# Performance work log

Hardware: AMD Instinct MI355X
Metric: run time of the kernel (lower is better)

Reference implementation:

```python
import jax, jax.numpy as jnp
import numpy as np

D = 3            # sheaf stalk dimension
HID = 128        # hidden_channels
OUT_SHAPE = (3, 3)
N_ROWS = 60000   # N_nodes * D
E = 960000       # edges (divisible by D)


def setup_inputs() -> dict:
    key = jax.random.key(0)
    k1, k2, k3 = jax.random.split(key, 3)
    x = jax.random.normal(k1, (N_ROWS, HID), dtype=jnp.float32)
    # nn.Linear(2*HID, prod(out_shape), bias=False): weight [out, in]
    W = jax.random.normal(k2, (int(np.prod(OUT_SHAPE)), 2 * HID), dtype=jnp.float32) * (1.0 / np.sqrt(2 * HID))
    edge_index = jax.random.randint(k3, (2, E), 0, N_ROWS, dtype=jnp.int64)
    return {"x": x, "W": W, "edge_index": edge_index}


def reference(x, W, edge_index):
    row, col = edge_index[0], edge_index[1]
    x_row = x[row]                                   # [E, HID] gather
    x_col = x[col]                                   # [E, HID] gather
    x_cat = jnp.concatenate([x_row, x_col], axis=-1) # [E, 2*HID]
    x_cat = x_cat.reshape(-1, D, 2 * HID).sum(axis=1)  # [E//D, 2*HID]
    maps = jnp.tanh(x_cat @ W.T)                     # [E//D, prod(out_shape)]
    return maps.reshape(-1, OUT_SHAPE[0], OUT_SHAPE[1])
```

## Files before the change

### kernel.cpp

```cpp
#include <hip/hip_runtime.h>
#include <hip/hip_fp16.h>
#include <math.h>

#define DD       3
#define HID      128
#define NOUT     9
#define N_ROWS_C 60000
#define NEDGE    960000
#define NGROUP   (NEDGE / DD)
#define YH_STRIDE 32

template <int CTRL>
__device__ __forceinline__ float dpp_xor_add(float v) {
    int r = __builtin_amdgcn_update_dpp(0, __float_as_int(v), CTRL, 0xf, 0xf, true);
    return v + __int_as_float(r);
}
__device__ __forceinline__ float red8(float v) {
    v = dpp_xor_add<0xB1>(v);
    v = dpp_xor_add<0x4E>(v);
    v = dpp_xor_add<0x141>(v);
    return v;
}

__device__ __forceinline__ float fast_tanh(float v) {
    float e = __builtin_amdgcn_exp2f(v * 2.8853900817779268f);
    return 1.0f - 2.0f * __builtin_amdgcn_rcpf(e + 1.0f);
}

__device__ __forceinline__ unsigned int pk(float a, float b) {
    __half2 h = __floats2half2_rn(a, b);
    return *reinterpret_cast<unsigned int*>(&h);
}

__global__ __launch_bounds__(256) void precompute_y(
    const float* __restrict__ x, const float* __restrict__ W, __half* __restrict__ yh)
{
    __shared__ float4 sW[576];
    const int t = threadIdx.x;
    const float4* __restrict__ Wv = reinterpret_cast<const float4*>(W);
    for (int i = t; i < 576; i += 256) sW[i] = Wv[i];

    const int s    = t & 7;
    const int slot = t >> 3;
    const int base = blockIdx.x * 64;
    const int r0   = base + slot;
    const int r1   = base + 32 + slot;
    const int r1c  = (r1 < N_ROWS_C) ? r1 : 0;

    __syncthreads();

    const float4* __restrict__ xv = reinterpret_cast<const float4*>(x);

    float aL0[NOUT], aR0[NOUT], aL1[NOUT], aR1[NOUT];
#pragma unroll
    for (int j = 0; j < NOUT; ++j) { aL0[j] = 0.f; aR0[j] = 0.f; aL1[j] = 0.f; aR1[j] = 0.f; }

#pragma unroll
    for (int q = 0; q < 4; ++q) {
        const int f = s + 8 * q;
        float4 x0 = xv[(size_t)r0  * 32 + f];
        float4 x1 = xv[(size_t)r1c * 32 + f];
#pragma unroll
        for (int j = 0; j < NOUT; ++j) {
            float4 wl = sW[j * 64 + f];
            float4 wr = sW[j * 64 + 32 + f];
            aL0[j] += x0.x * wl.x + x0.y * wl.y + x0.z * wl.z + x0.w * wl.w;
            aR0[j] += x0.x * wr.x + x0.y * wr.y + x0.z * wr.z + x0.w * wr.w;
            aL1[j] += x1.x * wl.x + x1.y * wl.y + x1.z * wl.z + x1.w * wl.w;
            aR1[j] += x1.x * wr.x + x1.y * wr.y + x1.z * wr.z + x1.w * wr.w;
        }
    }

#pragma unroll
    for (int j = 0; j < NOUT; ++j) {
        aL0[j] = red8(aL0[j]); aR0[j] = red8(aR0[j]);
        aL1[j] = red8(aL1[j]); aR1[j] = red8(aR1[j]);
    }

    if (s == 0) {
        __half* yr = yh + (size_t)r0 * YH_STRIDE;
        *reinterpret_cast<uint4*>(yr) =
            make_uint4(pk(aL0[0],aL0[1]), pk(aL0[2],aL0[3]), pk(aL0[4],aL0[5]), pk(aL0[6],aL0[7]));
        *reinterpret_cast<uint2*>(yr + 8)  = make_uint2(pk(aL0[8], 0.f), 0u);
        *reinterpret_cast<uint4*>(yr + 16) =
            make_uint4(pk(aR0[0],aR0[1]), pk(aR0[2],aR0[3]), pk(aR0[4],aR0[5]), pk(aR0[6],aR0[7]));
        *reinterpret_cast<uint2*>(yr + 24) = make_uint2(pk(aR0[8], 0.f), 0u);
    } else if (s == 1 && r1 < N_ROWS_C) {
        __half* yr = yh + (size_t)r1 * YH_STRIDE;
        *reinterpret_cast<uint4*>(yr) =
            make_uint4(pk(aL1[0],aL1[1]), pk(aL1[2],aL1[3]), pk(aL1[4],aL1[5]), pk(aL1[6],aL1[7]));
        *reinterpret_cast<uint2*>(yr + 8)  = make_uint2(pk(aL1[8], 0.f), 0u);
        *reinterpret_cast<uint4*>(yr + 16) =
            make_uint4(pk(aR1[0],aR1[1]), pk(aR1[2],aR1[3]), pk(aR1[4],aR1[5]), pk(aR1[6],aR1[7]));
        *reinterpret_cast<uint2*>(yr + 24) = make_uint2(pk(aR1[8], 0.f), 0u);
    }
}

__device__ __forceinline__ void acc9(float* a, uint4 v, unsigned int v4) {
    float2 f;
    f = __half22float2(*reinterpret_cast<__half2*>(&v.x)); a[0] += f.x; a[1] += f.y;
    f = __half22float2(*reinterpret_cast<__half2*>(&v.y)); a[2] += f.x; a[3] += f.y;
    f = __half22float2(*reinterpret_cast<__half2*>(&v.z)); a[4] += f.x; a[5] += f.y;
    f = __half22float2(*reinterpret_cast<__half2*>(&v.w)); a[6] += f.x; a[7] += f.y;
    f = __half22float2(*reinterpret_cast<__half2*>(&v4));  a[8] += f.x;
}

__global__ __launch_bounds__(256) void gather_tanh(
    const int* __restrict__ eidx, const __half* __restrict__ yh, float* __restrict__ out)
{
    __shared__ int   sRow[3 * 256];
    __shared__ int   sCol[3 * 256];
    __shared__ float sOut[NOUT * 256];

    const int t  = threadIdx.x;
    const int g0 = blockIdx.x * 256;
    const int e0 = g0 * 3;

#pragma unroll
    for (int p = 0; p < 3; ++p) {
        int e = e0 + t + p * 256;
        sRow[t + p * 256] = eidx[e];
        sCol[t + p * 256] = eidx[NEDGE + e];
    }
    __syncthreads();

    float a[NOUT];
#pragma unroll
    for (int j = 0; j < NOUT; ++j) a[j] = 0.f;

#pragma unroll
    for (int p = 0; p < 3; ++p) {
        {
            const unsigned int* pr =
                reinterpret_cast<const unsigned int*>(yh + (size_t)sRow[3 * t + p] * YH_STRIDE);
            uint4 v = *reinterpret_cast<const uint4*>(pr);
            unsigned int v4 = pr[4];
            acc9(a, v, v4);
        }
        {
            const unsigned int* pc =
                reinterpret_cast<const unsigned int*>(yh + (size_t)sCol[3 * t + p] * YH_STRIDE + 16);
            uint4 v = *reinterpret_cast<const uint4*>(pc);
            unsigned int v4 = pc[4];
            acc9(a, v, v4);
        }
    }

#pragma unroll
    for (int j = 0; j < NOUT; ++j) sOut[t * NOUT + j] = fast_tanh(a[j]);
    __syncthreads();

    float* o = out + (size_t)g0 * NOUT;
#pragma unroll
    for (int j = 0; j < NOUT; ++j) {
        o[t + 256 * j] = sOut[t + 256 * j];
    }
}

extern "C" void kernel_launch(void* const* d_in, const int* in_sizes, int n_in,
                              void* d_out, int out_size, void* d_ws, size_t ws_size,
                              hipStream_t stream) {
    const float* x    = (const float*)d_in[0];
    const float* W    = (const float*)d_in[1];
    const int*   eidx = (const int*)d_in[2];
    float*       out  = (float*)d_out;
    __half*      yh   = (__half*)d_ws;

    precompute_y<<<(N_ROWS_C + 63) / 64, 256, 0, stream>>>(x, W, yh);
    gather_tanh<<<NGROUP / 256, 256, 0, stream>>>(eidx, yh, out);
}
```

Measured before the change: 105.3 us.

## Fuse projection and gather into one cooperative kernel with grid sync

Merges the per-row projection pass and the edge gather/tanh pass into a single cooperative kernel launched with a fixed grid of 512 blocks. Each block loops over projection tiles, then all blocks meet at a grid-wide barrier and loop over edge chunks, reusing one shared-memory buffer for both phases. This aims to remove the second launch and the gap between the kernels. In exchange it adds a grid barrier, persistent-loop overhead, and a 512-block cap on parallelism. The two-kernel path is kept as a fallback if the cooperative launch fails.

```diff
diff --git a/kernel.cpp b/kernel.cpp
--- a/kernel.cpp
+++ b/kernel.cpp
@@ -1,13 +1,17 @@
 #include <hip/hip_runtime.h>
 #include <hip/hip_fp16.h>
+#include <hip/hip_cooperative_groups.h>
 #include <math.h>
 
-#define DD       3
-#define HID      128
-#define NOUT     9
-#define N_ROWS_C 60000
-#define NEDGE    960000
-#define NGROUP   (NEDGE / DD)
+namespace cg = cooperative_groups;
+
+#define NOUT      9
+#define N_ROWS_C  60000
+#define NEDGE     960000
+#define NGROUP    (NEDGE / 3)
+#define NCHUNK    (NGROUP / 256)
+#define NTILE     ((N_ROWS_C + 63) / 64)
+#define COOP_GRID 512
 #define YH_STRIDE 32
 
 template <int CTRL>
@@ -32,24 +36,25 @@
     return *reinterpret_cast<unsigned int*>(&h);
 }
 
-__global__ __launch_bounds__(256) void precompute_y(
-    const float* __restrict__ x, const float* __restrict__ W, __half* __restrict__ yh)
-{
-    __shared__ float4 sW[576];
-    const int t = threadIdx.x;
-    const float4* __restrict__ Wv = reinterpret_cast<const float4*>(W);
-    for (int i = t; i < 576; i += 256) sW[i] = Wv[i];
-
+__device__ __forceinline__ void acc9(float* a, uint4 v, unsigned int v4) {
+    float2 f;
+    f = __half22float2(*reinterpret_cast<__half2*>(&v.x)); a[0] += f.x; a[1] += f.y;
+    f = __half22float2(*reinterpret_cast<__half2*>(&v.y)); a[2] += f.x; a[3] += f.y;
+    f = __half22float2(*reinterpret_cast<__half2*>(&v.z)); a[4] += f.x; a[5] += f.y;
+    f = __half22float2(*reinterpret_cast<__half2*>(&v.w)); a[6] += f.x; a[7] += f.y;
+    f = __half22float2(*reinterpret_cast<__half2*>(&v4));  a[8] += f.x;
+}
+
+__device__ __forceinline__ void phaseA_tile(
+    const float4* __restrict__ xv, const float4* sW, int tile, int t,
+    __half* __restrict__ yh)
+{
     const int s    = t & 7;
     const int slot = t >> 3;
-    const int base = blockIdx.x * 64;
+    const int base = tile * 64;
     const int r0   = base + slot;
     const int r1   = base + 32 + slot;
     const int r1c  = (r1 < N_ROWS_C) ? r1 : 0;
-
-    __syncthreads();
-
-    const float4* __restrict__ xv = reinterpret_cast<const float4*>(x);
 
     float aL0[NOUT], aR0[NOUT], aL1[NOUT], aR1[NOUT];
 #pragma unroll
@@ -96,24 +101,12 @@
     }
 }
 
-__device__ __forceinline__ void acc9(float* a, uint4 v, unsigned int v4) {
-    float2 f;
-    f = __half22float2(*reinterpret_cast<__half2*>(&v.x)); a[0] += f.x; a[1] += f.y;
-    f = __half22float2(*reinterpret_cast<__half2*>(&v.y)); a[2] += f.x; a[3] += f.y;
-    f = __half22float2(*reinterpret_cast<__half2*>(&v.z)); a[4] += f.x; a[5] += f.y;
-    f = __half22float2(*reinterpret_cast<__half2*>(&v.w)); a[6] += f.x; a[7] += f.y;
-    f = __half22float2(*reinterpret_cast<__half2*>(&v4));  a[8] += f.x;
-}
-
-__global__ __launch_bounds__(256) void gather_tanh(
-    const int* __restrict__ eidx, const __half* __restrict__ yh, float* __restrict__ out)
-{
-    __shared__ int   sRow[3 * 256];
-    __shared__ int   sCol[3 * 256];
-    __shared__ float sOut[NOUT * 256];
-
-    const int t  = threadIdx.x;
-    const int g0 = blockIdx.x * 256;
+__device__ __forceinline__ void phaseB_chunk(
+    const int* __restrict__ eidx, const __half* __restrict__ yh,
+    float* __restrict__ out, int chunk, int t,
+    int* sRow, int* sCol, float* sOut)
+{
+    const int g0 = chunk * 256;
     const int e0 = g0 * 3;
 
 #pragma unroll
@@ -134,15 +127,13 @@
             const unsigned int* pr =
                 reinterpret_cast<const unsigned int*>(yh + (size_t)sRow[3 * t + p] * YH_STRIDE);
             uint4 v = *reinterpret_cast<const uint4*>(pr);
-            unsigned int v4 = pr[4];
-            acc9(a, v, v4);
+            acc9(a, v, pr[4]);
         }
         {
             const unsigned int* pc =
                 reinterpret_cast<const unsigned int*>(yh + (size_t)sCol[3 * t + p] * YH_STRIDE + 16);
             uint4 v = *reinterpret_cast<const uint4*>(pc);
-            unsigned int v4 = pc[4];
-            acc9(a, v, v4);
+            acc9(a, v, pc[4]);
         }
     }
 
@@ -155,6 +146,53 @@
     for (int j = 0; j < NOUT; ++j) {
         o[t + 256 * j] = sOut[t + 256 * j];
     }
+    __syncthreads();
+}
+
+__global__ __launch_bounds__(256, 2) void fused_sheaf(
+    const float* __restrict__ x, const float* __restrict__ W,
+    const int* __restrict__ eidx, __half* __restrict__ yh, float* __restrict__ out)
+{
+    __shared__ __align__(16) char smem[15360];
+    const int t = threadIdx.x;
+
+    float4* sW = reinterpret_cast<float4*>(smem);
+    const float4* __restrict__ Wv = reinterpret_cast<const float4*>(W);
+    for (int i = t; i < 576; i += 256) sW[i] = Wv[i];
+    __syncthreads();
+
+    const float4* __restrict__ xv = reinterpret_cast<const float4*>(x);
+    for (int tile = blockIdx.x; tile < NTILE; tile += COOP_GRID)
+        phaseA_tile(xv, sW, tile, t, yh);
+
+    cg::this_grid().sync();
+
+    int*   sRow = reinterpret_cast<int*>(smem);
+    int*   sCol = sRow + 768;
+    float* sOut = reinterpret_cast<float*>(sCol + 768);
+
+    for (int chunk = blockIdx.x; chunk < NCHUNK; chunk += COOP_GRID)
+        phaseB_chunk(eidx, yh, out, chunk, t, sRow, sCol, sOut);
+}
+
+__global__ __launch_bounds__(256) void precompute_y(
+    const float* __restrict__ x, const float* __restrict__ W, __half* __restrict__ yh)
+{
+    __shared__ float4 sW[576];
+    const int t = threadIdx.x;
+    const float4* __restrict__ Wv = reinterpret_cast<const float4*>(W);
+    for (int i = t; i < 576; i += 256) sW[i] = Wv[i];
+    __syncthreads();
+    phaseA_tile(reinterpret_cast<const float4*>(x), sW, blockIdx.x, t, yh);
+}
+
+__global__ __launch_bounds__(256) void gather_tanh(
+    const int* __restrict__ eidx, const __half* __restrict__ yh, float* __restrict__ out)
+{
+    __shared__ int   sRow[3 * 256];
+    __shared__ int   sCol[3 * 256];
+    __shared__ float sOut[NOUT * 256];
+    phaseB_chunk(eidx, yh, out, blockIdx.x, threadIdx.x, sRow, sCol, sOut);
 }
 
 extern "C" void kernel_launch(void* const* d_in, const int* in_sizes, int n_in,
@@ -166,6 +204,11 @@
     float*       out  = (float*)d_out;
     __half*      yh   = (__half*)d_ws;
 
-    precompute_y<<<(N_ROWS_C + 63) / 64, 256, 0, stream>>>(x, W, yh);
-    gather_tanh<<<NGROUP / 256, 256, 0, stream>>>(eidx, yh, out);
-}
+    void* args[] = { (void*)&x, (void*)&W, (void*)&eidx, (void*)&yh, (void*)&out };
+    hipError_t err = hipLaunchCooperativeKernel(
+        reinterpret_cast<void*>(fused_sheaf), dim3(COOP_GRID), dim3(256), args, 0, stream);
+    if (err != hipSuccess) {
+        precompute_y<<<NTILE, 256, 0, stream>>>(x, W, yh);
+        gather_tanh<<<NCHUNK, 256, 0, stream>>>(eidx, yh, out);
+    }
+}
```

Measured after the change: 234.2 us. +122.5%, slower.
